# Kernel tuning notes

Measured on AMD Instinct MI355X. Metric: run time of the kernel, lower is better.

The kernel has to match this reference:

```python
import jax, jax.numpy as jnp
import numpy as np

# db4 decomposition low-pass filter, pywt coefficient order
DEC_LO = np.array([-0.010597401784997278, 0.032883011666982945,
                   0.030841381835986965, -0.18703481171888114,
                   -0.02798376941698385, 0.6308807679295904,
                   0.7148465705525415, 0.23037781330885523], dtype=np.float32)
LEVEL = 5
B, C, L = 64, 64, 8192


def _qmf_hi(dec_lo):
    # pywt relation: dec_hi[n] = (-1)^(n+1) * dec_lo[F-1-n]
    F = dec_lo.shape[0]
    signs = jnp.where(jnp.arange(F) % 2 == 0, -1.0, 1.0).astype(dec_lo.dtype)
    return signs * dec_lo[::-1]


def _wavedec(x, dec_lo, dec_hi):
    # pywt.dwt(v, w, 'symmetric') == np.convolve(sym_pad(v, F-1), filt, 'valid')[1::2]
    # implemented as a stride-2 cross-correlation with the reversed filter.
    b, c, n = x.shape
    v = x.reshape(b * c, n)
    F = dec_lo.shape[0]
    # kernel: (out_ch=2 [lo, hi], in_ch=1, width=F); reversed => true convolution
    k = jnp.stack([dec_lo[::-1], dec_hi[::-1]])[:, None, :]
    details = []
    for _ in range(LEVEL):
        ext = jnp.pad(v, ((0, 0), (F - 1, F - 1)), mode='symmetric')[:, 1:]
        y = jax.lax.conv_general_dilated(ext[:, None, :], k,
                                         window_strides=(2,), padding='VALID')
        v = y[:, 0, :]           # approximation -> next level input
        details.append(y[:, 1, :])  # detail for this level (finest first)
    approx = v.reshape(b, c, -1)
    # pywt order: [cA_L, cD_L, ..., cD_1] -> coarsest detail first
    det = [d.reshape(b, c, -1) for d in reversed(details)]
    return (approx, *det)


def setup_inputs() -> dict:
    key = jax.random.key(0)
    x = jax.random.normal(key, (B, C, L), dtype=jnp.float32)
    dec_lo = jnp.asarray(DEC_LO)
    dec_hi = _qmf_hi(dec_lo)
    return {"x": x, "dec_lo": dec_lo, "dec_hi": dec_hi}


def reference(x, dec_lo, dec_hi):
    # Returns (cA_L, cD_L, cD_{L-1}, ..., cD_1), matching the torch module's
    # [approx_tensor, detail_tensors] flattened.
    return _wavedec(x, dec_lo, dec_hi)
```

## Files before the change

kernel.cpp:

```cpp
#include <hip/hip_runtime.h>


static constexpr int ROWS = 4096;
static constexpr int N0 = 8192;
static constexpr int L1n = 4099, L2n = 2053, L3n = 1030, L4n = 518, L5n = 262;
static constexpr size_t OFF_D5 = 1073152u;
static constexpr size_t OFF_D4 = 2146304u;
static constexpr size_t OFF_D3 = 4268032u;
static constexpr size_t OFF_D2 = 8486912u;
static constexpr size_t OFF_D1 = 16896000u;

__device__ __forceinline__ int physidx(int i) { return i + (i >> 3); }

template <bool SRCPAD, bool DSTPAD>
__device__ __forceinline__ void dwt_level(
    const float* __restrict__ src, int n, int m,
    const float* __restrict__ h, const float* __restrict__ g,
    float* __restrict__ adst, float* __restrict__ ddst, int tid)
{
    const int ngroups = (m + 3) >> 2;
    const int jin_max = (n - 10) >> 3;
    for (int j = tid; j < ngroups; j += 256) {
        const int p0 = 4 * j;
        if (j >= 1 && j <= jin_max && p0 + 3 < m) {
            float w[16];
            if (SRCPAD) {
                const float* __restrict__ p = src + (9 * j - 7);
                w[0] = p[0];  w[1] = p[1];  w[2] = p[2];  w[3] = p[3];
                w[4] = p[4];  w[5] = p[5];
                w[6] = p[7];  w[7] = p[8];  w[8] = p[9];  w[9] = p[10];
                w[10] = p[11]; w[11] = p[12]; w[12] = p[13]; w[13] = p[14];
                w[14] = p[16]; w[15] = p[17];
            } else {
                const float2* __restrict__ s2 =
                    reinterpret_cast<const float2*>(src + (8 * j - 6));
#pragma unroll
                for (int t = 0; t < 8; ++t) {
                    const float2 v = s2[t];
                    w[2 * t] = v.x; w[2 * t + 1] = v.y;
                }
            }
            float aa[4], dd[4];
#pragma unroll
            for (int r = 0; r < 4; ++r) {
                float a = 0.f, d = 0.f;
#pragma unroll
                for (int q = 0; q < 8; ++q) {
                    const float v = w[2 * r + 7 - q];
                    a = fmaf(h[q], v, a);
                    d = fmaf(g[q], v, d);
                }
                aa[r] = a; dd[r] = d;
            }
            if (DSTPAD) {
                float* __restrict__ q4 = adst + (4 * j + (j >> 1));
#pragma unroll
                for (int r = 0; r < 4; ++r) q4[r] = aa[r];
            } else {
#pragma unroll
                for (int r = 0; r < 4; ++r) adst[p0 + r] = aa[r];
            }
#pragma unroll
            for (int r = 0; r < 4; ++r) ddst[p0 + r] = dd[r];
        } else {
#pragma unroll 4
            for (int r = 0; r < 4; ++r) {
                const int pos = p0 + r;
                if (pos >= m) break;
                const int s0 = 2 * pos + 1;
                float a = 0.f, d = 0.f;
#pragma unroll
                for (int q = 0; q < 8; ++q) {
                    int s = s0 - q;
                    int idx = (s < 0) ? (-1 - s) : ((s >= n) ? (2 * n - 1 - s) : s);
                    const float v = SRCPAD ? src[physidx(idx)] : src[idx];
                    a = fmaf(h[q], v, a);
                    d = fmaf(g[q], v, d);
                }
                ddst[pos] = d;
                if (DSTPAD) adst[physidx(pos)] = a;
                else        adst[pos] = a;
            }
        }
    }
}

__global__ __launch_bounds__(256, 5)
void wavedec5_kernel(const float* __restrict__ x,
                     const float* __restrict__ dlo,
                     const float* __restrict__ dhi,
                     float* __restrict__ out)
{
    __shared__ __align__(16) float bufA[4612];
    __shared__ __align__(16) float bufB[2312];

    const int row = blockIdx.x;
    const int tid = threadIdx.x;

    float h[8], g[8];
#pragma unroll
    for (int i = 0; i < 8; ++i) { h[i] = dlo[i]; g[i] = dhi[i]; }

    const float* __restrict__ xr = x + (size_t)row * N0;

    dwt_level<false, true>(xr, N0, L1n, h, g, bufA,
                           out + OFF_D1 + (size_t)row * L1n, tid);
    __syncthreads();
    dwt_level<true, true>(bufA, L1n, L2n, h, g, bufB,
                          out + OFF_D2 + (size_t)row * L2n, tid);
    __syncthreads();
    dwt_level<true, true>(bufB, L2n, L3n, h, g, bufA,
                          out + OFF_D3 + (size_t)row * L3n, tid);
    __syncthreads();
    dwt_level<true, true>(bufA, L3n, L4n, h, g, bufB,
                          out + OFF_D4 + (size_t)row * L4n, tid);
    __syncthreads();
    dwt_level<true, false>(bufB, L4n, L5n, h, g,
                           out + (size_t)row * L5n,
                           out + OFF_D5 + (size_t)row * L5n, tid);
}

extern "C" void kernel_launch(void* const* d_in, const int* in_sizes, int n_in,
                              void* d_out, int out_size, void* d_ws, size_t ws_size,
                              hipStream_t stream) {
    const float* x   = (const float*)d_in[0];
    const float* dlo = (const float*)d_in[1];
    const float* dhi = (const float*)d_in[2];
    float* out = (float*)d_out;
    wavedec5_kernel<<<ROWS, 256, 0, stream>>>(x, dlo, dhi, out);
}
```

Measured before the change: 64.10 us.

## Drop padded LDS layout, use float4 loads and stores, raise occupancy hint

Removes the bank-conflict padding (i + i/8) from the shared-memory buffers so each thread reads its input window with five 16-byte vector loads from an aligned offset and writes approximation and detail outputs as float4 stores. Smaller LDS buffers and a launch_bounds minimum of 6 blocks per CU aim for higher occupancy and fewer load/store instructions. In exchange, unpadded LDS accesses with a stride of 8 floats per thread may cause bank conflicts. The detail stores go to global rows whose lengths are odd, so those float4 stores are only 4-byte aligned, which may split them.

```diff
diff --git a/kernel.cpp b/kernel.cpp
--- a/kernel.cpp
+++ b/kernel.cpp
@@ -10,58 +10,42 @@
 static constexpr size_t OFF_D2 = 8486912u;
 static constexpr size_t OFF_D1 = 16896000u;
 
-__device__ __forceinline__ int physidx(int i) { return i + (i >> 3); }
+typedef float f4 __attribute__((ext_vector_type(4)));
+typedef f4 f4a __attribute__((aligned(4)));
 
-template <bool SRCPAD, bool DSTPAD>
+template <bool LAST>
 __device__ __forceinline__ void dwt_level(
     const float* __restrict__ src, int n, int m,
     const float* __restrict__ h, const float* __restrict__ g,
     float* __restrict__ adst, float* __restrict__ ddst, int tid)
 {
     const int ngroups = (m + 3) >> 2;
-    const int jin_max = (n - 10) >> 3;
+    const int jmax = (n - 12) >> 3;
     for (int j = tid; j < ngroups; j += 256) {
         const int p0 = 4 * j;
-        if (j >= 1 && j <= jin_max && p0 + 3 < m) {
-            float w[16];
-            if (SRCPAD) {
-                const float* __restrict__ p = src + (9 * j - 7);
-                w[0] = p[0];  w[1] = p[1];  w[2] = p[2];  w[3] = p[3];
-                w[4] = p[4];  w[5] = p[5];
-                w[6] = p[7];  w[7] = p[8];  w[8] = p[9];  w[9] = p[10];
-                w[10] = p[11]; w[11] = p[12]; w[12] = p[13]; w[13] = p[14];
-                w[14] = p[16]; w[15] = p[17];
-            } else {
-                const float2* __restrict__ s2 =
-                    reinterpret_cast<const float2*>(src + (8 * j - 6));
+        if (j >= 1 && j <= jmax && p0 + 3 < m) {
+            const f4* __restrict__ s4 = reinterpret_cast<const f4*>(src + (8 * j - 8));
+            f4 vv[5];
 #pragma unroll
-                for (int t = 0; t < 8; ++t) {
-                    const float2 v = s2[t];
-                    w[2 * t] = v.x; w[2 * t + 1] = v.y;
-                }
-            }
-            float aa[4], dd[4];
+            for (int t = 0; t < 5; ++t) vv[t] = s4[t];
+            float W[20];
+#pragma unroll
+            for (int i = 0; i < 20; ++i) W[i] = vv[i >> 2][i & 3];
+            f4 aa, dd;
 #pragma unroll
             for (int r = 0; r < 4; ++r) {
                 float a = 0.f, d = 0.f;
 #pragma unroll
                 for (int q = 0; q < 8; ++q) {
-                    const float v = w[2 * r + 7 - q];
+                    const float v = W[2 * r + 9 - q];
                     a = fmaf(h[q], v, a);
                     d = fmaf(g[q], v, d);
                 }
                 aa[r] = a; dd[r] = d;
             }
-            if (DSTPAD) {
-                float* __restrict__ q4 = adst + (4 * j + (j >> 1));
-#pragma unroll
-                for (int r = 0; r < 4; ++r) q4[r] = aa[r];
-            } else {
-#pragma unroll
-                for (int r = 0; r < 4; ++r) adst[p0 + r] = aa[r];
-            }
-#pragma unroll
-            for (int r = 0; r < 4; ++r) ddst[p0 + r] = dd[r];
+            *reinterpret_cast<f4a*>(ddst + p0) = dd;
+            if (LAST) *reinterpret_cast<f4a*>(adst + p0) = aa;
+            else      *reinterpret_cast<f4*>(adst + p0) = aa;
         } else {
 #pragma unroll 4
             for (int r = 0; r < 4; ++r) {
@@ -73,26 +57,25 @@
                 for (int q = 0; q < 8; ++q) {
                     int s = s0 - q;
                     int idx = (s < 0) ? (-1 - s) : ((s >= n) ? (2 * n - 1 - s) : s);
-                    const float v = SRCPAD ? src[physidx(idx)] : src[idx];
+                    const float v = src[idx];
                     a = fmaf(h[q], v, a);
                     d = fmaf(g[q], v, d);
                 }
                 ddst[pos] = d;
-                if (DSTPAD) adst[physidx(pos)] = a;
-                else        adst[pos] = a;
+                adst[pos] = a;
             }
         }
     }
 }
 
-__global__ __launch_bounds__(256, 5)
+__global__ __launch_bounds__(256, 6)
 void wavedec5_kernel(const float* __restrict__ x,
                      const float* __restrict__ dlo,
                      const float* __restrict__ dhi,
                      float* __restrict__ out)
 {
-    __shared__ __align__(16) float bufA[4612];
-    __shared__ __align__(16) float bufB[2312];
+    __shared__ __align__(16) float bufA[4100];
+    __shared__ __align__(16) float bufB[2056];
 
     const int row = blockIdx.x;
     const int tid = threadIdx.x;
@@ -103,21 +86,21 @@
 
     const float* __restrict__ xr = x + (size_t)row * N0;
 
-    dwt_level<false, true>(xr, N0, L1n, h, g, bufA,
-                           out + OFF_D1 + (size_t)row * L1n, tid);
+    dwt_level<false>(xr, N0, L1n, h, g, bufA,
+                     out + OFF_D1 + (size_t)row * L1n, tid);
     __syncthreads();
-    dwt_level<true, true>(bufA, L1n, L2n, h, g, bufB,
-                          out + OFF_D2 + (size_t)row * L2n, tid);
+    dwt_level<false>(bufA, L1n, L2n, h, g, bufB,
+                     out + OFF_D2 + (size_t)row * L2n, tid);
     __syncthreads();
-    dwt_level<true, true>(bufB, L2n, L3n, h, g, bufA,
-                          out + OFF_D3 + (size_t)row * L3n, tid);
+    dwt_level<false>(bufB, L2n, L3n, h, g, bufA,
+                     out + OFF_D3 + (size_t)row * L3n, tid);
     __syncthreads();
-    dwt_level<true, true>(bufA, L3n, L4n, h, g, bufB,
-                          out + OFF_D4 + (size_t)row * L4n, tid);
+    dwt_level<false>(bufA, L3n, L4n, h, g, bufB,
+                     out + OFF_D4 + (size_t)row * L4n, tid);
     __syncthreads();
-    dwt_level<true, false>(bufB, L4n, L5n, h, g,
-                           out + (size_t)row * L5n,
-                           out + OFF_D5 + (size_t)row * L5n, tid);
+    dwt_level<true>(bufB, L4n, L5n, h, g,
+                    out + (size_t)row * L5n,
+                    out + OFF_D5 + (size_t)row * L5n, tid);
 }
 
 extern "C" void kernel_launch(void* const* d_in, const int* in_sizes, int n_in,
```

After: 66.67 us. 1.04x slower.

## Move intermediate levels to per-wave global workspace, one row per wavefront

Applied to the files above, without the earlier changes.

Adds a path where each 64-lane wavefront handles one row and keeps intermediate approximation buffers in a global workspace instead of LDS, so no block-wide barriers are needed and LDS no longer limits occupancy. The LDS fallback drops the bank-conflict padding scheme and shrinks its buffers, allowing a higher occupancy hint. The workspace path adds global memory traffic for the intermediates (likely mostly cached in L2) and reads from global rather than LDS.

```diff
diff --git a/kernel.cpp b/kernel.cpp
--- a/kernel.cpp
+++ b/kernel.cpp
@@ -10,35 +10,28 @@
 static constexpr size_t OFF_D2 = 8486912u;
 static constexpr size_t OFF_D1 = 16896000u;
 
-__device__ __forceinline__ int physidx(int i) { return i + (i >> 3); }
+static constexpr int WS_B = 4104;
+static constexpr int WS_STRIDE = 6160;
+static constexpr size_t WS_NEED = (size_t)ROWS * WS_STRIDE * sizeof(float);
 
-template <bool SRCPAD, bool DSTPAD>
+template <int STRIDE>
 __device__ __forceinline__ void dwt_level(
     const float* __restrict__ src, int n, int m,
     const float* __restrict__ h, const float* __restrict__ g,
     float* __restrict__ adst, float* __restrict__ ddst, int tid)
 {
     const int ngroups = (m + 3) >> 2;
-    const int jin_max = (n - 10) >> 3;
-    for (int j = tid; j < ngroups; j += 256) {
+    const int jmax = (n - 10) >> 3;
+    for (int j = tid; j < ngroups; j += STRIDE) {
         const int p0 = 4 * j;
-        if (j >= 1 && j <= jin_max && p0 + 3 < m) {
+        if (j >= 1 && j <= jmax && p0 + 3 < m) {
+            const float2* __restrict__ s2 =
+                reinterpret_cast<const float2*>(src) + (4 * j - 3);
             float w[16];
-            if (SRCPAD) {
-                const float* __restrict__ p = src + (9 * j - 7);
-                w[0] = p[0];  w[1] = p[1];  w[2] = p[2];  w[3] = p[3];
-                w[4] = p[4];  w[5] = p[5];
-                w[6] = p[7];  w[7] = p[8];  w[8] = p[9];  w[9] = p[10];
-                w[10] = p[11]; w[11] = p[12]; w[12] = p[13]; w[13] = p[14];
-                w[14] = p[16]; w[15] = p[17];
-            } else {
-                const float2* __restrict__ s2 =
-                    reinterpret_cast<const float2*>(src + (8 * j - 6));
 #pragma unroll
-                for (int t = 0; t < 8; ++t) {
-                    const float2 v = s2[t];
-                    w[2 * t] = v.x; w[2 * t + 1] = v.y;
-                }
+            for (int t = 0; t < 8; ++t) {
+                const float2 v = s2[t];
+                w[2 * t] = v.x; w[2 * t + 1] = v.y;
             }
             float aa[4], dd[4];
 #pragma unroll
@@ -52,16 +45,10 @@
                 }
                 aa[r] = a; dd[r] = d;
             }
-            if (DSTPAD) {
-                float* __restrict__ q4 = adst + (4 * j + (j >> 1));
-#pragma unroll
-                for (int r = 0; r < 4; ++r) q4[r] = aa[r];
-            } else {
-#pragma unroll
-                for (int r = 0; r < 4; ++r) adst[p0 + r] = aa[r];
-            }
 #pragma unroll
             for (int r = 0; r < 4; ++r) ddst[p0 + r] = dd[r];
+#pragma unroll
+            for (int r = 0; r < 4; ++r) adst[p0 + r] = aa[r];
         } else {
 #pragma unroll 4
             for (int r = 0; r < 4; ++r) {
@@ -73,26 +60,51 @@
                 for (int q = 0; q < 8; ++q) {
                     int s = s0 - q;
                     int idx = (s < 0) ? (-1 - s) : ((s >= n) ? (2 * n - 1 - s) : s);
-                    const float v = SRCPAD ? src[physidx(idx)] : src[idx];
+                    const float v = src[idx];
                     a = fmaf(h[q], v, a);
                     d = fmaf(g[q], v, d);
                 }
                 ddst[pos] = d;
-                if (DSTPAD) adst[physidx(pos)] = a;
-                else        adst[pos] = a;
+                adst[pos] = a;
             }
         }
     }
 }
 
-__global__ __launch_bounds__(256, 5)
-void wavedec5_kernel(const float* __restrict__ x,
-                     const float* __restrict__ dlo,
-                     const float* __restrict__ dhi,
-                     float* __restrict__ out)
+__global__ __launch_bounds__(256)
+void wavedec5_ws(const float* __restrict__ x,
+                 const float* __restrict__ dlo,
+                 const float* __restrict__ dhi,
+                 float* __restrict__ out,
+                 float* __restrict__ ws)
 {
-    __shared__ __align__(16) float bufA[4612];
-    __shared__ __align__(16) float bufB[2312];
+    const int lane = threadIdx.x & 63;
+    const int row  = (blockIdx.x << 2) + (threadIdx.x >> 6);
+
+    float h[8], g[8];
+#pragma unroll
+    for (int i = 0; i < 8; ++i) { h[i] = dlo[i]; g[i] = dhi[i]; }
+
+    const float* __restrict__ xr = x + (size_t)row * N0;
+    float* bufA = ws + (size_t)row * WS_STRIDE;
+    float* bufB = bufA + WS_B;
+
+    dwt_level<64>(xr,   N0,  L1n, h, g, bufA, out + OFF_D1 + (size_t)row * L1n, lane);
+    dwt_level<64>(bufA, L1n, L2n, h, g, bufB, out + OFF_D2 + (size_t)row * L2n, lane);
+    dwt_level<64>(bufB, L2n, L3n, h, g, bufA, out + OFF_D3 + (size_t)row * L3n, lane);
+    dwt_level<64>(bufA, L3n, L4n, h, g, bufB, out + OFF_D4 + (size_t)row * L4n, lane);
+    dwt_level<64>(bufB, L4n, L5n, h, g,
+                  out + (size_t)row * L5n, out + OFF_D5 + (size_t)row * L5n, lane);
+}
+
+__global__ __launch_bounds__(256, 6)
+void wavedec5_lds(const float* __restrict__ x,
+                  const float* __restrict__ dlo,
+                  const float* __restrict__ dhi,
+                  float* __restrict__ out)
+{
+    __shared__ __align__(16) float bufA[4100];
+    __shared__ __align__(16) float bufB[2056];
 
     const int row = blockIdx.x;
     const int tid = threadIdx.x;
@@ -103,21 +115,16 @@
 
     const float* __restrict__ xr = x + (size_t)row * N0;
 
-    dwt_level<false, true>(xr, N0, L1n, h, g, bufA,
-                           out + OFF_D1 + (size_t)row * L1n, tid);
+    dwt_level<256>(xr,   N0,  L1n, h, g, bufA, out + OFF_D1 + (size_t)row * L1n, tid);
     __syncthreads();
-    dwt_level<true, true>(bufA, L1n, L2n, h, g, bufB,
-                          out + OFF_D2 + (size_t)row * L2n, tid);
+    dwt_level<256>(bufA, L1n, L2n, h, g, bufB, out + OFF_D2 + (size_t)row * L2n, tid);
     __syncthreads();
-    dwt_level<true, true>(bufB, L2n, L3n, h, g, bufA,
-                          out + OFF_D3 + (size_t)row * L3n, tid);
+    dwt_level<256>(bufB, L2n, L3n, h, g, bufA, out + OFF_D3 + (size_t)row * L3n, tid);
     __syncthreads();
-    dwt_level<true, true>(bufA, L3n, L4n, h, g, bufB,
-                          out + OFF_D4 + (size_t)row * L4n, tid);
+    dwt_level<256>(bufA, L3n, L4n, h, g, bufB, out + OFF_D4 + (size_t)row * L4n, tid);
     __syncthreads();
-    dwt_level<true, false>(bufB, L4n, L5n, h, g,
-                           out + (size_t)row * L5n,
-                           out + OFF_D5 + (size_t)row * L5n, tid);
+    dwt_level<256>(bufB, L4n, L5n, h, g,
+                   out + (size_t)row * L5n, out + OFF_D5 + (size_t)row * L5n, tid);
 }
 
 extern "C" void kernel_launch(void* const* d_in, const int* in_sizes, int n_in,
@@ -127,5 +134,9 @@
     const float* dlo = (const float*)d_in[1];
     const float* dhi = (const float*)d_in[2];
     float* out = (float*)d_out;
-    wavedec5_kernel<<<ROWS, 256, 0, stream>>>(x, dlo, dhi, out);
+    if (ws_size >= WS_NEED && d_ws != nullptr) {
+        wavedec5_ws<<<ROWS / 4, 256, 0, stream>>>(x, dlo, dhi, out, (float*)d_ws);
+    } else {
+        wavedec5_lds<<<ROWS, 256, 0, stream>>>(x, dlo, dhi, out);
+    }
 }
```

Measured after the change: 112.5 us. 75.5% more time.
